# Performance work log

Measured on AMD Instinct MI355X. Metric: run time of the kernel, lower is better.

Reference implementation:

```python
import jax, jax.numpy as jnp
import numpy as np

NUM_FREQS = 8
TEMPERATURE = 100.0
DOWNSAMPLE = 64
GRID = 8
D_OUT = 512


def fourier_embed(x):
    # x: [M, 2] -> [M, NUM_FREQS*2*2], order: per freq [sin(f*x), cos(f*x)]
    freqs = TEMPERATURE ** (jnp.arange(NUM_FREQS, dtype=jnp.float32) / NUM_FREQS)
    xf = x[:, None, :] * freqs[None, :, None]  # [M, F, 2]
    feats = jnp.stack([jnp.sin(xf), jnp.cos(xf)], axis=2)  # [M, F, 2, 2]
    return feats.reshape(x.shape[0], -1)  # [M, 32]


def mlp(x, W1, b1, W2, b2, W3, b3):
    h = jax.nn.silu(x @ W1 + b1)
    h = jax.nn.silu(h @ W2 + b2)
    return h @ W3 + b3


def scatter_to_grid(drags, emb):
    # drags: [BV, N, 2] (pixel coords), emb: [BV, N, 512]
    BV, N, _ = drags.shape
    r = drags[..., 0].astype(jnp.int32) // DOWNSAMPLE  # [BV, N]
    c = drags[..., 1].astype(jnp.int32) // DOWNSAMPLE
    idx = r * GRID + c  # flat cell index in [0, 64)
    b_idx = jnp.arange(BV)[:, None]
    grid = jnp.zeros((BV, GRID * GRID, D_OUT), emb.dtype).at[b_idx, idx].add(emb)
    # -> [BV, 512, 8, 8]
    return grid.transpose(0, 2, 1).reshape(BV, D_OUT, GRID, GRID)


def setup_inputs() -> dict:
    key = jax.random.key(0)
    ks = jax.random.split(key, 8)
    B, V, N = 8, 8, 1024
    IMG = GRID * DOWNSAMPLE  # 512
    drags_start = jax.random.uniform(ks[0], (B, V, N, 2), jnp.float32) * IMG
    drags_end = jax.random.uniform(ks[1], (B, V, N, 2), jnp.float32) * IMG
    pd = NUM_FREQS * 2 * 2  # 32
    W1 = jax.random.normal(ks[2], (pd, 128), jnp.float32) * (1.0 / np.sqrt(pd))
    b1 = jnp.zeros((128,), jnp.float32)
    W2 = jax.random.normal(ks[3], (128, 256), jnp.float32) * (1.0 / np.sqrt(128))
    b2 = jnp.zeros((256,), jnp.float32)
    W3 = jax.random.normal(ks[4], (256, 512), jnp.float32) * (1.0 / np.sqrt(256))
    b3 = jnp.zeros((512,), jnp.float32)
    return dict(drags_start=drags_start, drags_end=drags_end,
                W1=W1, b1=b1, W2=W2, b2=b2, W3=W3, b3=b3)


def reference(drags_start, drags_end, W1, b1, W2, b2, W3, b3):
    B, V, N, _ = drags_start.shape
    BV = B * V
    ds = drags_start.reshape(BV, N, 2)
    de = drags_end.reshape(BV, N, 2)

    def embed(d):  # [BV, N, 2] -> [BV, N, 512]
        feats = fourier_embed(d.reshape(BV * N, 2))  # no_grad in torch
        return mlp(feats, W1, b1, W2, b2, W3, b3).reshape(BV, N, D_OUT)

    emb_s = embed(ds)
    emb_e = embed(de)
    merge_s = scatter_to_grid(ds, emb_s)
    merge_e = scatter_to_grid(de, emb_e)
    return jnp.concatenate([merge_s, merge_e], axis=1)  # [BV, 1024, 8, 8]
```

## Files before the change

### kernel.cpp

```cpp
#include <hip/hip_runtime.h>
#include <hip/hip_bf16.h>

typedef _Float16 half8 __attribute__((ext_vector_type(8)));
typedef _Float16 half4v __attribute__((ext_vector_type(4)));
typedef float floatx4 __attribute__((ext_vector_type(4)));
typedef unsigned int uint2v __attribute__((ext_vector_type(2)));

__device__ const float FREQS[8] = {
    1.0f, 1.7782794100389228f, 3.1622776601683795f, 5.623413251903491f,
    10.0f, 17.78279410038923f, 31.622776601683793f, 56.23413251903491f};

__device__ inline void fsincos(float m, float& s, float& c) {
  constexpr double I2PI_D = 0.15915494309189533576888376337251;
  constexpr float HI = (float)I2PI_D;
  constexpr float LO = (float)(I2PI_D - (double)HI);
  float k = rintf(m * HI);
  float f = fmaf(m, HI, -k);
  f = fmaf(m, LO, f);
  s = __builtin_amdgcn_sinf(f);
  c = __builtin_amdgcn_cosf(f);
}

__device__ inline float fsilu(float x) {
  return x * __builtin_amdgcn_rcpf(1.f + __expf(-x));
}

__global__ __launch_bounds__(256) void prep_weights(
    const float* __restrict__ W1, const float* __restrict__ W2,
    const float* __restrict__ W3, _Float16* __restrict__ W1t,
    _Float16* __restrict__ W2t, _Float16* __restrict__ W3f) {
  int tid = blockIdx.x * blockDim.x + threadIdx.x;
  int stride = gridDim.x * blockDim.x;
  for (int i = tid; i < 128 * 32; i += stride) {
    int n = i >> 5, k = i & 31;
    W1t[i] = (_Float16)W1[k * 128 + n];
  }
  for (int i = tid; i < 256 * 128; i += stride) {
    int n = i >> 7, k = i & 127;
    W2t[i] = (_Float16)W2[k * 256 + n];
  }
  for (int i = tid; i < 512 * 256; i += stride) {
    int k = i >> 9, n = i & 511;
    int it = n >> 4, ln = n & 15, ks = k >> 5, q = (k >> 3) & 3, j = k & 7;
    W3f[((size_t)(it * 8 + ks) * 64 + q * 16 + ln) * 8 + j] = (_Float16)W3[i];
  }
}

#define HS 136
__global__ __launch_bounds__(512, 4) void embed_scatter(
    const float* __restrict__ dstart, const float* __restrict__ dend,
    const float* __restrict__ b1, const float* __restrict__ b2,
    const _Float16* __restrict__ W1t, const _Float16* __restrict__ W2t,
    _Float16* __restrict__ swz, int* __restrict__ counts) {
  __shared__ _Float16 h1t[128 * HS];
  __shared__ _Float16 W1lds[4096];
  __shared__ float b1lds[128];
  __shared__ unsigned char cellb[128];
  __shared__ int hist[64];

  int bid = blockIdx.x;
  int bv = bid >> 3, tsel = (bid >> 2) & 1, pg = bid & 3;
  const float* src = tsel ? dend : dstart;
  int tid = threadIdx.x;
  int lane = tid & 63, w = tid >> 6, ln = lane & 15, q = lane >> 4;

  *(half8*)&W1lds[tid * 8] = *(const half8*)&W1t[tid * 8];
  if (tid < 128) b1lds[tid] = b1[tid];
  if (tid < 64) hist[tid] = 0;

  half8 w2f[2][4];
  float b2v[2];
  for (int nt = 0; nt < 2; nt++) {
    int n = w * 32 + nt * 16 + ln;
    b2v[nt] = b2[n];
    for (int ks = 0; ks < 4; ks++)
      w2f[nt][ks] = *(const half8*)&W2t[n * 128 + ks * 32 + q * 8];
  }
  floatx4 sacc[4][2];
  for (int mc = 0; mc < 4; mc++)
    for (int nt = 0; nt < 2; nt++) sacc[mc][nt] = (floatx4){0.f, 0.f, 0.f, 0.f};

  float fA = FREQS[2 * q], fB = FREQS[2 * q + 1];
  int pbase = bv * 1024 + pg * 256;
  __syncthreads();

  for (int c = 0; c < 2; c++) {
    int pl = c * 128 + w * 16 + ln;
    float2 xy = *(const float2*)&src[(size_t)(pbase + pl) * 2];
    if (q == 0) {
      int cell = ((int)xy.x >> 6) * 8 + ((int)xy.y >> 6);
      cellb[w * 16 + ln] = (unsigned char)cell;
      atomicAdd(&hist[cell], 1);
    }
    half8 fb;
    {
      float s, cc2;
      fsincos(xy.x * fA, s, cc2); fb[0] = (_Float16)s; fb[2] = (_Float16)cc2;
      fsincos(xy.y * fA, s, cc2); fb[1] = (_Float16)s; fb[3] = (_Float16)cc2;
      fsincos(xy.x * fB, s, cc2); fb[4] = (_Float16)s; fb[6] = (_Float16)cc2;
      fsincos(xy.y * fB, s, cc2); fb[5] = (_Float16)s; fb[7] = (_Float16)cc2;
    }
    for (int mtW = 0; mtW < 8; mtW++) {
      half8 w1f = *(const half8*)&W1lds[(mtW * 16 + ln) * 32 + q * 8];
      floatx4 c1 = *(const floatx4*)&b1lds[mtW * 16 + q * 4];
      c1 = __builtin_amdgcn_mfma_f32_16x16x32_f16(w1f, fb, c1, 0, 0, 0);
      half4v hv;
      for (int r = 0; r < 4; r++) hv[r] = (_Float16)fsilu(c1[r]);
      *(half4v*)&h1t[(w * 16 + ln) * HS + mtW * 16 + q * 4] = hv;
    }
    __syncthreads();
    for (int mt = 0; mt < 8; mt++) {
      half8 af[4];
      for (int ks = 0; ks < 4; ks++)
        af[ks] = *(const half8*)&h1t[(mt * 16 + ln) * HS + ks * 32 + q * 8];
      unsigned cw = *(const unsigned*)&cellb[mt * 16 + q * 4];
      unsigned c0 = cw & 255, c1i = (cw >> 8) & 255, c2i = (cw >> 16) & 255, c3i = cw >> 24;
      half4v ao[4];
      for (int mc = 0; mc < 4; mc++) {
        unsigned m = mc * 16 + ln;
        unsigned d0 = (c0 == m ? 0x3C00u : 0u) | (c1i == m ? 0x3C000000u : 0u);
        unsigned d1 = (c2i == m ? 0x3C00u : 0u) | (c3i == m ? 0x3C000000u : 0u);
        uint2v u = {d0, d1};
        ao[mc] = __builtin_bit_cast(half4v, u);
      }
      for (int nt = 0; nt < 2; nt++) {
        floatx4 cc = {b2v[nt], b2v[nt], b2v[nt], b2v[nt]};
        for (int ks = 0; ks < 4; ks++)
          cc = __builtin_amdgcn_mfma_f32_16x16x32_f16(af[ks], w2f[nt][ks], cc, 0, 0, 0);
        half4v hb;
        for (int r = 0; r < 4; r++) hb[r] = (_Float16)fsilu(cc[r]);
        for (int mc = 0; mc < 4; mc++)
          sacc[mc][nt] = __builtin_amdgcn_mfma_f32_16x16x16f16(ao[mc], hb, sacc[mc][nt], 0, 0, 0);
      }
    }
    __syncthreads();
  }
  for (int mc = 0; mc < 4; mc++)
    for (int nt = 0; nt < 2; nt++) {
      half4v hv;
      for (int r = 0; r < 4; r++) hv[r] = (_Float16)sacc[mc][nt][r];
      *(half4v*)&swz[((((size_t)bid * 4 + mc) * 16 + w * 2 + nt) * 64 + lane) * 4] = hv;
    }
  if (tid < 64) counts[bid * 64 + tid] = hist[tid];
}

#define AS 264
__global__ __launch_bounds__(256) void layer3(
    const _Float16* __restrict__ swz, const int* __restrict__ counts,
    const _Float16* __restrict__ W3f, const float* __restrict__ b3,
    float* __restrict__ out) {
  __shared__ _Float16 a_lds[16 * AS];
  __shared__ float cnt_s[16];
  int bb = blockIdx.x;
  int bvts = bb >> 2, cq = bb & 3;
  int tid = threadIdx.x;
  for (int it = 0; it < 4; it++) {
    int cc = it * 256 + tid;
    int wn = cc >> 6, lane2 = cc & 63, q2 = lane2 >> 4, ln2 = lane2 & 15;
    size_t base = ((size_t)bvts * 16 + cq) * 1024 + cc;
    half4v s = (*(const half4v*)&swz[base * 4] +
                *(const half4v*)&swz[(base + 4096) * 4]) +
               (*(const half4v*)&swz[(base + 8192) * 4] +
                *(const half4v*)&swz[(base + 12288) * 4]);
    int col = wn * 16 + ln2;
    for (int r = 0; r < 4; r++) a_lds[(q2 * 4 + r) * AS + col] = s[r];
  }
  if (tid < 16) {
    int base = bvts * 4 * 64 + cq * 16 + tid;
    cnt_s[tid] = (float)(counts[base] + counts[base + 64] +
                         counts[base + 128] + counts[base + 192]);
  }
  __syncthreads();
  int lane = tid & 63, w = tid >> 6, ln = lane & 15, q = lane >> 4;
  half8 af[8];
  for (int ks = 0; ks < 8; ks++)
    af[ks] = *(const half8*)&a_lds[ln * AS + ks * 32 + q * 8];
  float cntf = cnt_s[ln];
  for (int ii = 0; ii < 8; ii++) {
    int i = w * 8 + ii;
    half8 wf[8];
    for (int ks = 0; ks < 8; ks++)
      wf[ks] = *(const half8*)&W3f[((size_t)(i * 8 + ks) * 64 + lane) * 8];
    floatx4 b3v = *(const floatx4*)&b3[i * 16 + q * 4];
    floatx4 acc = {0.f, 0.f, 0.f, 0.f};
    for (int ks = 0; ks < 8; ks++)
      acc = __builtin_amdgcn_mfma_f32_16x16x32_f16(wf[ks], af[ks], acc, 0, 0, 0);
    for (int r = 0; r < 4; r++)
      out[((size_t)bvts * 512 + i * 16 + q * 4 + r) * 64 + cq * 16 + ln] =
          acc[r] + cntf * b3v[r];
  }
}

extern "C" void kernel_launch(void* const* d_in, const int* in_sizes, int n_in,
                              void* d_out, int out_size, void* d_ws, size_t ws_size,
                              hipStream_t stream) {
  const float* dstart = (const float*)d_in[0];
  const float* dend = (const float*)d_in[1];
  const float* W1 = (const float*)d_in[2];
  const float* b1 = (const float*)d_in[3];
  const float* W2 = (const float*)d_in[4];
  const float* b2 = (const float*)d_in[5];
  const float* W3 = (const float*)d_in[6];
  const float* b3 = (const float*)d_in[7];
  float* out = (float*)d_out;

  char* ws = (char*)d_ws;
  _Float16* W1t = (_Float16*)(ws);
  _Float16* W2t = (_Float16*)(ws + 8192);
  _Float16* W3f = (_Float16*)(ws + 73728);
  _Float16* swz = (_Float16*)(ws + 335872);
  int* counts = (int*)(ws + 335872 + 16777216);

  hipLaunchKernelGGL(prep_weights, dim3(64), dim3(256), 0, stream,
                     W1, W2, W3, W1t, W2t, W3f);
  hipLaunchKernelGGL(embed_scatter, dim3(512), dim3(512), 0, stream,
                     dstart, dend, b1, b2, W1t, W2t, swz, counts);
  hipLaunchKernelGGL(layer3, dim3(512), dim3(256), 0, stream,
                     swz, counts, W3f, b3, out);
}
```

Before: 119.1 us.

## Precompute one-hot scatter fragments, use K=32 scatter MFMA, retile layer3 for reuse

embed_scatter now computes cell indices and the histogram up front and builds the one-hot scatter operands once into shared memory. The scatter GEMM moves from 16x16x16 to 16x16x32 MFMA by processing two 16-point tiles per step, and layer-1 output is stored in a fragment-swizzled layout instead of a padded one. layer3 is retiled so each block covers all 64 cells for one bv/type and a quarter of the output channels. Each loaded W3 fragment is then reused across four cell tiles, which aims to cut redundant W3 reads and halve scatter MFMA count. The cost is more shared memory per block, which may lower occupancy.

```diff
diff --git a/kernel.cpp b/kernel.cpp
--- a/kernel.cpp
+++ b/kernel.cpp
@@ -4,7 +4,7 @@
 typedef _Float16 half8 __attribute__((ext_vector_type(8)));
 typedef _Float16 half4v __attribute__((ext_vector_type(4)));
 typedef float floatx4 __attribute__((ext_vector_type(4)));
-typedef unsigned int uint2v __attribute__((ext_vector_type(2)));
+typedef unsigned int uint4v __attribute__((ext_vector_type(4)));
 
 __device__ const float FREQS[8] = {
     1.0f, 1.7782794100389228f, 3.1622776601683795f, 5.623413251903491f,
@@ -46,16 +46,16 @@
   }
 }
 
-#define HS 136
 __global__ __launch_bounds__(512, 4) void embed_scatter(
     const float* __restrict__ dstart, const float* __restrict__ dend,
     const float* __restrict__ b1, const float* __restrict__ b2,
     const _Float16* __restrict__ W1t, const _Float16* __restrict__ W2t,
     _Float16* __restrict__ swz, int* __restrict__ counts) {
-  __shared__ _Float16 h1t[128 * HS];
+  __shared__ _Float16 h1f[16384];
   __shared__ _Float16 W1lds[4096];
+  __shared__ _Float16 ohs[8192];
   __shared__ float b1lds[128];
-  __shared__ unsigned char cellb[128];
+  __shared__ unsigned char cellb[256];
   __shared__ int hist[64];
 
   int bid = blockIdx.x;
@@ -67,6 +67,15 @@
   *(half8*)&W1lds[tid * 8] = *(const half8*)&W1t[tid * 8];
   if (tid < 128) b1lds[tid] = b1[tid];
   if (tid < 64) hist[tid] = 0;
+  __syncthreads();
+
+  int pbase = bv * 1024 + pg * 256;
+  if (tid < 256) {
+    float2 xy = *(const float2*)&src[(size_t)(pbase + tid) * 2];
+    int cell = ((int)xy.x >> 6) * 8 + ((int)xy.y >> 6);
+    cellb[tid] = (unsigned char)cell;
+    atomicAdd(&hist[cell], 1);
+  }
 
   half8 w2f[2][4];
   float b2v[2];
@@ -81,17 +90,25 @@
     for (int nt = 0; nt < 2; nt++) sacc[mc][nt] = (floatx4){0.f, 0.f, 0.f, 0.f};
 
   float fA = FREQS[2 * q], fB = FREQS[2 * q + 1];
-  int pbase = bv * 1024 + pg * 256;
   __syncthreads();
 
   for (int c = 0; c < 2; c++) {
+    for (int e = 0; e < 2; e++) {
+      int eid = tid * 2 + e;
+      int l2 = eid & 63, mc = (eid >> 6) & 3, tt = eid >> 8;
+      unsigned m = (unsigned)(mc * 16 + (l2 & 15));
+      int pb = c * 128 + tt * 32 + (l2 >> 4) * 4;
+      unsigned ca = *(const unsigned*)&cellb[pb];
+      unsigned cb = *(const unsigned*)&cellb[pb + 16];
+      unsigned d0 = ((ca & 255) == m ? 0x3C00u : 0u) | (((ca >> 8) & 255) == m ? 0x3C000000u : 0u);
+      unsigned d1 = (((ca >> 16) & 255) == m ? 0x3C00u : 0u) | ((ca >> 24) == m ? 0x3C000000u : 0u);
+      unsigned d2 = ((cb & 255) == m ? 0x3C00u : 0u) | (((cb >> 8) & 255) == m ? 0x3C000000u : 0u);
+      unsigned d3 = (((cb >> 16) & 255) == m ? 0x3C00u : 0u) | ((cb >> 24) == m ? 0x3C000000u : 0u);
+      uint4v u = {d0, d1, d2, d3};
+      *(half8*)&ohs[eid * 8] = __builtin_bit_cast(half8, u);
+    }
     int pl = c * 128 + w * 16 + ln;
     float2 xy = *(const float2*)&src[(size_t)(pbase + pl) * 2];
-    if (q == 0) {
-      int cell = ((int)xy.x >> 6) * 8 + ((int)xy.y >> 6);
-      cellb[w * 16 + ln] = (unsigned char)cell;
-      atomicAdd(&hist[cell], 1);
-    }
     half8 fb;
     {
       float s, cc2;
@@ -106,31 +123,33 @@
       c1 = __builtin_amdgcn_mfma_f32_16x16x32_f16(w1f, fb, c1, 0, 0, 0);
       half4v hv;
       for (int r = 0; r < 4; r++) hv[r] = (_Float16)fsilu(c1[r]);
-      *(half4v*)&h1t[(w * 16 + ln) * HS + mtW * 16 + q * 4] = hv;
+      int addr = (((w * 4 + (mtW >> 1)) * 4 + ((mtW & 1) * 2 + (q >> 1))) * 16 + ln) * 8 + (q & 1) * 4;
+      *(half4v*)&h1f[addr] = hv;
     }
     __syncthreads();
-    for (int mt = 0; mt < 8; mt++) {
-      half8 af[4];
-      for (int ks = 0; ks < 4; ks++)
-        af[ks] = *(const half8*)&h1t[(mt * 16 + ln) * HS + ks * 32 + q * 8];
-      unsigned cw = *(const unsigned*)&cellb[mt * 16 + q * 4];
-      unsigned c0 = cw & 255, c1i = (cw >> 8) & 255, c2i = (cw >> 16) & 255, c3i = cw >> 24;
-      half4v ao[4];
-      for (int mc = 0; mc < 4; mc++) {
-        unsigned m = mc * 16 + ln;
-        unsigned d0 = (c0 == m ? 0x3C00u : 0u) | (c1i == m ? 0x3C000000u : 0u);
-        unsigned d1 = (c2i == m ? 0x3C00u : 0u) | (c3i == m ? 0x3C000000u : 0u);
-        uint2v u = {d0, d1};
-        ao[mc] = __builtin_bit_cast(half4v, u);
+    for (int t = 0; t < 4; t++) {
+      half8 af0[4], af1[4];
+      for (int ks = 0; ks < 4; ks++) {
+        af0[ks] = *(const half8*)&h1f[((((2 * t) * 4 + ks) * 4 + q) * 16 + ln) * 8];
+        af1[ks] = *(const half8*)&h1f[((((2 * t + 1) * 4 + ks) * 4 + q) * 16 + ln) * 8];
       }
+      half8 oh[4];
+      for (int mc = 0; mc < 4; mc++)
+        oh[mc] = *(const half8*)&ohs[((t * 4 + mc) * 64 + lane) * 8];
       for (int nt = 0; nt < 2; nt++) {
-        floatx4 cc = {b2v[nt], b2v[nt], b2v[nt], b2v[nt]};
-        for (int ks = 0; ks < 4; ks++)
-          cc = __builtin_amdgcn_mfma_f32_16x16x32_f16(af[ks], w2f[nt][ks], cc, 0, 0, 0);
-        half4v hb;
-        for (int r = 0; r < 4; r++) hb[r] = (_Float16)fsilu(cc[r]);
+        floatx4 c0 = {b2v[nt], b2v[nt], b2v[nt], b2v[nt]};
+        floatx4 c1 = c0;
+        for (int ks = 0; ks < 4; ks++) {
+          c0 = __builtin_amdgcn_mfma_f32_16x16x32_f16(af0[ks], w2f[nt][ks], c0, 0, 0, 0);
+          c1 = __builtin_amdgcn_mfma_f32_16x16x32_f16(af1[ks], w2f[nt][ks], c1, 0, 0, 0);
+        }
+        half8 hb;
+        for (int r = 0; r < 4; r++) {
+          hb[r] = (_Float16)fsilu(c0[r]);
+          hb[4 + r] = (_Float16)fsilu(c1[r]);
+        }
         for (int mc = 0; mc < 4; mc++)
-          sacc[mc][nt] = __builtin_amdgcn_mfma_f32_16x16x16f16(ao[mc], hb, sacc[mc][nt], 0, 0, 0);
+          sacc[mc][nt] = __builtin_amdgcn_mfma_f32_16x16x32_f16(oh[mc], hb, sacc[mc][nt], 0, 0, 0);
       }
     }
     __syncthreads();
@@ -144,50 +163,58 @@
   if (tid < 64) counts[bid * 64 + tid] = hist[tid];
 }
 
-#define AS 264
 __global__ __launch_bounds__(256) void layer3(
     const _Float16* __restrict__ swz, const int* __restrict__ counts,
     const _Float16* __restrict__ W3f, const float* __restrict__ b3,
     float* __restrict__ out) {
-  __shared__ _Float16 a_lds[16 * AS];
-  __shared__ float cnt_s[16];
-  int bb = blockIdx.x;
-  int bvts = bb >> 2, cq = bb & 3;
+  __shared__ _Float16 bfrag[16384];
+  __shared__ float cnt_s[64];
+  int bvts = blockIdx.x;
+  int ch2 = blockIdx.y;
   int tid = threadIdx.x;
-  for (int it = 0; it < 4; it++) {
-    int cc = it * 256 + tid;
-    int wn = cc >> 6, lane2 = cc & 63, q2 = lane2 >> 4, ln2 = lane2 & 15;
-    size_t base = ((size_t)bvts * 16 + cq) * 1024 + cc;
+  for (int it = 0; it < 16; it++) {
+    int idx = it * 256 + tid;
+    int mc = idx >> 10, wnt = (idx >> 6) & 15, l = idx & 63;
+    int qq = l >> 4, lnn = l & 15;
+    size_t base = (size_t)bvts * 16384 + (size_t)idx;
     half4v s = (*(const half4v*)&swz[base * 4] +
                 *(const half4v*)&swz[(base + 4096) * 4]) +
                (*(const half4v*)&swz[(base + 8192) * 4] +
                 *(const half4v*)&swz[(base + 12288) * 4]);
-    int col = wn * 16 + ln2;
-    for (int r = 0; r < 4; r++) a_lds[(q2 * 4 + r) * AS + col] = s[r];
-  }
-  if (tid < 16) {
-    int base = bvts * 4 * 64 + cq * 16 + tid;
+    int abase = ((mc * 8 + (wnt >> 1)) * 4 + ((wnt & 1) * 2 + (lnn >> 3))) * 16;
+    for (int r = 0; r < 4; r++)
+      bfrag[(abase + qq * 4 + r) * 8 + (lnn & 7)] = s[r];
+  }
+  if (tid < 64) {
+    int base = bvts * 256 + tid;
     cnt_s[tid] = (float)(counts[base] + counts[base + 64] +
                          counts[base + 128] + counts[base + 192]);
   }
   __syncthreads();
   int lane = tid & 63, w = tid >> 6, ln = lane & 15, q = lane >> 4;
-  half8 af[8];
-  for (int ks = 0; ks < 8; ks++)
-    af[ks] = *(const half8*)&a_lds[ln * AS + ks * 32 + q * 8];
-  float cntf = cnt_s[ln];
-  for (int ii = 0; ii < 8; ii++) {
-    int i = w * 8 + ii;
-    half8 wf[8];
-    for (int ks = 0; ks < 8; ks++)
-      wf[ks] = *(const half8*)&W3f[((size_t)(i * 8 + ks) * 64 + lane) * 8];
-    floatx4 b3v = *(const floatx4*)&b3[i * 16 + q * 4];
-    floatx4 acc = {0.f, 0.f, 0.f, 0.f};
-    for (int ks = 0; ks < 8; ks++)
-      acc = __builtin_amdgcn_mfma_f32_16x16x32_f16(wf[ks], af[ks], acc, 0, 0, 0);
-    for (int r = 0; r < 4; r++)
-      out[((size_t)bvts * 512 + i * 16 + q * 4 + r) * 64 + cq * 16 + ln] =
-          acc[r] + cntf * b3v[r];
+  floatx4 acc[2][4];
+  for (int i2 = 0; i2 < 2; i2++)
+    for (int cn = 0; cn < 4; cn++) acc[i2][cn] = (floatx4){0.f, 0.f, 0.f, 0.f};
+  for (int ks = 0; ks < 8; ks++) {
+    half8 bf[4];
+    for (int cn = 0; cn < 4; cn++)
+      bf[cn] = *(const half8*)&bfrag[(((cn * 8 + ks) * 4 + q) * 16 + ln) * 8];
+    for (int i2 = 0; i2 < 2; i2++) {
+      int I = ch2 * 8 + w * 2 + i2;
+      half8 wf = *(const half8*)&W3f[(size_t)((I * 8 + ks) * 64 + lane) * 8];
+      for (int cn = 0; cn < 4; cn++)
+        acc[i2][cn] = __builtin_amdgcn_mfma_f32_16x16x32_f16(wf, bf[cn], acc[i2][cn], 0, 0, 0);
+    }
+  }
+  for (int i2 = 0; i2 < 2; i2++) {
+    int nb = ch2 * 128 + (w * 2 + i2) * 16;
+    floatx4 b3v = *(const floatx4*)&b3[nb + q * 4];
+    for (int cn = 0; cn < 4; cn++) {
+      float cf = cnt_s[cn * 16 + ln];
+      for (int r = 0; r < 4; r++)
+        out[((size_t)bvts * 512 + nb + q * 4 + r) * 64 + cn * 16 + ln] =
+            acc[i2][cn][r] + cf * b3v[r];
+    }
   }
 }
 
@@ -215,6 +242,6 @@
                      W1, W2, W3, W1t, W2t, W3f);
   hipLaunchKernelGGL(embed_scatter, dim3(512), dim3(512), 0, stream,
                      dstart, dend, b1, b2, W1t, W2t, swz, counts);
-  hipLaunchKernelGGL(layer3, dim3(512), dim3(256), 0, stream,
+  hipLaunchKernelGGL(layer3, dim3(128, 4), dim3(256), 0, stream,
                      swz, counts, W3f, b3, out);
 }
```

Measured after the change: 128.4 us. 1.08x slower.
